# Kernel tuning notes

Measured on AMD Instinct MI355X. Metric: run time of the kernel, lower is better.

Reference implementation:

```python
import jax, jax.numpy as jnp
import numpy as np

N_NODES = 50000
N_EDGES = 800000
IN_DIM = 256
OUT_DIM = 256


def setup_inputs() -> dict:
    key = jax.random.key(0)
    k1, k2, k3, k4, k5, k6 = jax.random.split(key, 6)
    x = jax.random.normal(k1, (N_NODES, IN_DIM), dtype=jnp.float32)
    adj_rows = jax.random.randint(k2, (N_EDGES,), 0, N_NODES)
    adj_cols = jax.random.randint(k3, (N_EDGES,), 0, N_NODES)
    adj_vals = jax.random.uniform(k4, (N_EDGES,), dtype=jnp.float32)
    stdv = 1.0 / np.sqrt(OUT_DIM)
    W = jax.random.uniform(k5, (IN_DIM, OUT_DIM), minval=-stdv, maxval=stdv, dtype=jnp.float32)
    b = jax.random.uniform(k6, (OUT_DIM,), minval=-stdv, maxval=stdv, dtype=jnp.float32)
    return {"x": x, "adj_rows": adj_rows, "adj_cols": adj_cols, "adj_vals": adj_vals, "W": W, "b": b}


def reference(x, adj_rows, adj_cols, adj_vals, W, b):
    # hidden = x @ W  (first sparse.mm; x treated dense, identical math)
    hidden = jnp.matmul(x, W)  # [N, out_dim]
    # output = adj @ hidden via COO SpMM: gather source rows, scale, scatter-add to dest rows
    msgs = adj_vals[:, None] * hidden[adj_cols]  # [E, out_dim]
    output = jax.ops.segment_sum(msgs, adj_rows, num_segments=N_NODES)  # [N, out_dim]
    return output + b
```

## Files before the change

kernel.cpp:

```cpp
#include <hip/hip_runtime.h>

#define N_NODES 50000
#define N_EDGES 800000
#define DIM     256
#define STRIPS32 1563
#define NBLK_NODES 196
#define GEMM_BLOCKS 196
#define COUNT_BLOCKS 782
#define K2_BLOCKS (GEMM_BLOCKS + COUNT_BLOCKS)

typedef __attribute__((ext_vector_type(8))) short bf16x8;
typedef __attribute__((ext_vector_type(4))) float f32x4;

__device__ __forceinline__ unsigned short f2bf(float f) {
    unsigned u = __float_as_uint(f);
    unsigned r = (u + 0x7fffu + ((u >> 16) & 1u)) >> 16;
    return (unsigned short)r;
}
__device__ __forceinline__ float bf2f(unsigned short h) {
    return __uint_as_float((unsigned)h << 16);
}

__device__ __forceinline__ int block_excl_scan_256(int v, int* wsum, int* total) {
    const int lane = threadIdx.x & 63;
    const int wave = threadIdx.x >> 6;
    int x = v;
#pragma unroll
    for (int off = 1; off < 64; off <<= 1) {
        const int y = __shfl_up(x, off, 64);
        if (lane >= off) x += y;
    }
    if (lane == 63) wsum[wave] = x;
    __syncthreads();
    if (threadIdx.x == 0) {
        int s = 0;
#pragma unroll
        for (int w = 0; w < 4; ++w) { const int t = wsum[w]; wsum[w] = s; s += t; }
        *total = s;
    }
    __syncthreads();
    return wsum[wave] + x - v;
}

__global__ __launch_bounds__(256)
void prep(const float* __restrict__ W, unsigned short* __restrict__ Wt,
          int* __restrict__ cntcur) {
    const int i = blockIdx.x * 256 + threadIdx.x;
    if (i < 2 * N_NODES) cntcur[i] = 0;
    if (blockIdx.x < DIM) {
        const int n = blockIdx.x, k = threadIdx.x;
        Wt[n * DIM + k] = f2bf(W[(size_t)k * DIM + n]);
    }
}

__global__ __launch_bounds__(512, 2)
void gemm_count(const float* __restrict__ X, const unsigned short* __restrict__ Wt,
                unsigned short* __restrict__ Hb,
                const int* __restrict__ rows, int* __restrict__ cnt) {
    __shared__ unsigned short wl[DIM * DIM];
    const int tid = threadIdx.x;

    if (blockIdx.x >= GEMM_BLOCKS) {
        const int base = (blockIdx.x - GEMM_BLOCKS) * 1024;
        int e = base + tid;
        if (e < N_EDGES) atomicAdd(&cnt[rows[e]], 1);
        e += 512;
        if (e < N_EDGES) atomicAdd(&cnt[rows[e]], 1);
        return;
    }

    {
        const uint4* src = (const uint4*)Wt;
#pragma unroll
        for (int i = 0; i < 16; ++i) {
            const int c   = i * 512 + tid;
            const int row = c >> 5;
            const int kb  = (c & 31) * 16;
            const int dst = row * 512 + (kb ^ ((row & 7) << 4));
            *(uint4*)((char*)wl + dst) = src[c];
        }
    }
    __syncthreads();

    const int wid   = tid >> 6;
    const int lane  = tid & 63;
    const int strip = blockIdx.x * 8 + wid;
    if (strip >= STRIPS32) return;

    const int r0   = strip * 32;
    const int arow = lane & 15;
    const int kgrp = lane >> 4;
    const int ra = r0 + arow;
    const int rb = r0 + 16 + arow;
    const float* xa = X + (size_t)(ra < N_NODES ? ra : N_NODES - 1) * DIM + kgrp * 8;
    const float* xb = X + (size_t)(rb < N_NODES ? rb : N_NODES - 1) * DIM + kgrp * 8;

    f32x4 acc[2][16];
#pragma unroll
    for (int h = 0; h < 2; ++h)
#pragma unroll
        for (int nt = 0; nt < 16; ++nt) acc[h][nt] = f32x4{0.f, 0.f, 0.f, 0.f};

    const int swz = (arow & 7) << 4;

    float4 pa0 = *(const float4*)(xa);
    float4 pa1 = *(const float4*)(xa + 4);
    float4 pb0 = *(const float4*)(xb);
    float4 pb1 = *(const float4*)(xb + 4);

#pragma unroll
    for (int ks = 0; ks < 8; ++ks) {
        bf16x8 a0, a1;
        a0[0] = (short)f2bf(pa0.x); a0[1] = (short)f2bf(pa0.y);
        a0[2] = (short)f2bf(pa0.z); a0[3] = (short)f2bf(pa0.w);
        a0[4] = (short)f2bf(pa1.x); a0[5] = (short)f2bf(pa1.y);
        a0[6] = (short)f2bf(pa1.z); a0[7] = (short)f2bf(pa1.w);
        a1[0] = (short)f2bf(pb0.x); a1[1] = (short)f2bf(pb0.y);
        a1[2] = (short)f2bf(pb0.z); a1[3] = (short)f2bf(pb0.w);
        a1[4] = (short)f2bf(pb1.x); a1[5] = (short)f2bf(pb1.y);
        a1[6] = (short)f2bf(pb1.z); a1[7] = (short)f2bf(pb1.w);
        if (ks < 7) {
            pa0 = *(const float4*)(xa + (ks + 1) * 32);
            pa1 = *(const float4*)(xa + (ks + 1) * 32 + 4);
            pb0 = *(const float4*)(xb + (ks + 1) * 32);
            pb1 = *(const float4*)(xb + (ks + 1) * 32 + 4);
        }
        const int kb = ((ks * 32 + kgrp * 8) * 2) ^ swz;
#pragma unroll
        for (int nt = 0; nt < 16; ++nt) {
            const int n = nt * 16 + arow;
            const bf16x8 b = *(const bf16x8*)((const char*)wl + n * 512 + kb);
            acc[0][nt] = __builtin_amdgcn_mfma_f32_16x16x32_bf16(a0, b, acc[0][nt], 0, 0, 0);
            acc[1][nt] = __builtin_amdgcn_mfma_f32_16x16x32_bf16(a1, b, acc[1][nt], 0, 0, 0);
        }
    }

#pragma unroll
    for (int h = 0; h < 2; ++h) {
        const int crow0 = r0 + h * 16 + kgrp * 4;
#pragma unroll
        for (int nt = 0; nt < 16; ++nt) {
#pragma unroll
            for (int q = 0; q < 4; ++q) {
                const int r = crow0 + q;
                if (r < N_NODES)
                    Hb[(size_t)r * DIM + nt * 16 + arow] = f2bf(acc[h][nt][q]);
            }
        }
    }
}

__global__ __launch_bounds__(256)
void scan_blocks(const int* __restrict__ cnt, int* __restrict__ offs,
                 int* __restrict__ bsum) {
    __shared__ int wsum[4];
    __shared__ int total;
    const int i = blockIdx.x * 256 + threadIdx.x;
    const int v = (i < N_NODES) ? cnt[i] : 0;
    const int excl = block_excl_scan_256(v, wsum, &total);
    if (i < N_NODES) offs[i] = excl;
    if (threadIdx.x == 0) bsum[blockIdx.x] = total;
}

__global__ __launch_bounds__(256)
void fill_edges(const int* __restrict__ rows, const int* __restrict__ cols,
                const float* __restrict__ vals, const int* __restrict__ offs,
                const int* __restrict__ bsum, int* __restrict__ cursor,
                int2* __restrict__ pe) {
    __shared__ int wsum[4];
    __shared__ int total;
    __shared__ int P[256];
    {
        const int t = threadIdx.x;
        const int v = (t < NBLK_NODES) ? bsum[t] : 0;
        const int excl = block_excl_scan_256(v, wsum, &total);
        P[t] = excl;
    }
    __syncthreads();
    const int e = blockIdx.x * 256 + threadIdx.x;
    if (e >= N_EDGES) return;
    const int r = rows[e];
    const int p = atomicAdd(&cursor[r], 1);
    pe[offs[r] + P[r >> 8] + p] = make_int2(cols[e], __float_as_int(vals[e]));
}

__global__ __launch_bounds__(256)
void spmm(const unsigned short* __restrict__ Hb, const int* __restrict__ offs,
          const int* __restrict__ bsum, const int2* __restrict__ pe,
          const float* __restrict__ bias, float* __restrict__ out) {
    __shared__ int wsum[4];
    __shared__ int total;
    __shared__ int P[256];
    {
        const int t = threadIdx.x;
        const int v = (t < NBLK_NODES) ? bsum[t] : 0;
        const int excl = block_excl_scan_256(v, wsum, &total);
        P[t] = excl;
    }
    __syncthreads();

    const int row  = blockIdx.x * 4 + (threadIdx.x >> 6);
    const int lane = threadIdx.x & 63;
    const int beg = offs[row] + P[row >> 8];
    const int end = (row + 1 == N_NODES) ? N_EDGES : (offs[row + 1] + P[(row + 1) >> 8]);
    const unsigned lb = (unsigned)lane * 4;
    float4 acc = make_float4(0.f, 0.f, 0.f, 0.f);
    int i = beg;
    for (; i + 8 <= end; i += 8) {
        int2 e[8];
#pragma unroll
        for (int j = 0; j < 8; ++j) e[j] = pe[i + j];
        ushort4 h[8];
#pragma unroll
        for (int j = 0; j < 8; ++j)
            h[j] = *(const ushort4*)&Hb[((unsigned)e[j].x << 8) + lb];
#pragma unroll
        for (int j = 0; j < 8; ++j) {
            const float v = __int_as_float(e[j].y);
            acc.x += v * bf2f(h[j].x);
            acc.y += v * bf2f(h[j].y);
            acc.z += v * bf2f(h[j].z);
            acc.w += v * bf2f(h[j].w);
        }
    }
    for (; i < end; ++i) {
        const int2 e0 = pe[i];
        const ushort4 h0 = *(const ushort4*)&Hb[((unsigned)e0.x << 8) + lb];
        const float v0 = __int_as_float(e0.y);
        acc.x += v0 * bf2f(h0.x);
        acc.y += v0 * bf2f(h0.y);
        acc.z += v0 * bf2f(h0.z);
        acc.w += v0 * bf2f(h0.w);
    }
    const float4 bb = *(const float4*)&bias[lane * 4];
    acc.x += bb.x; acc.y += bb.y; acc.z += bb.z; acc.w += bb.w;
    *(float4*)&out[(size_t)row * DIM + lane * 4] = acc;
}

extern "C" void kernel_launch(void* const* d_in, const int* in_sizes, int n_in,
                              void* d_out, int out_size, void* d_ws, size_t ws_size,
                              hipStream_t stream) {
    const float* x        = (const float*)d_in[0];
    const int*   adj_rows = (const int*)d_in[1];
    const int*   adj_cols = (const int*)d_in[2];
    const float* adj_vals = (const float*)d_in[3];
    const float* W        = (const float*)d_in[4];
    const float* b        = (const float*)d_in[5];
    float*       out      = (float*)d_out;

    char* ws = (char*)d_ws;
    size_t off = 0;
    auto alloc = [&](size_t bytes) {
        void* p = ws + off;
        off = (off + bytes + 255) & ~(size_t)255;
        return p;
    };
    unsigned short* hiddenb = (unsigned short*)alloc((size_t)N_NODES * DIM * sizeof(unsigned short));
    unsigned short* Wt      = (unsigned short*)alloc((size_t)DIM * DIM * sizeof(unsigned short));
    int*   offs    = (int*)  alloc((size_t)N_NODES * sizeof(int));
    int*   cntcur  = (int*)  alloc((size_t)2 * N_NODES * sizeof(int));
    int*   bsum    = (int*)  alloc(256 * sizeof(int));
    int2*  pe      = (int2*) alloc((size_t)N_EDGES * sizeof(int2));
    int* cnt    = cntcur;
    int* cursor = cntcur + N_NODES;

    prep<<<(2 * N_NODES + 255) / 256, 256, 0, stream>>>(W, Wt, cntcur);

    gemm_count<<<K2_BLOCKS, 512, 0, stream>>>(x, Wt, hiddenb, adj_rows, cnt);

    scan_blocks<<<NBLK_NODES, 256, 0, stream>>>(cnt, offs, bsum);

    fill_edges<<<(N_EDGES + 255) / 256, 256, 0, stream>>>(
        adj_rows, adj_cols, adj_vals, offs, bsum, cursor, pe);

    spmm<<<N_NODES / 4, 256, 0, stream>>>(hiddenb, offs, bsum, pe, b, out);
}
```

Measured before the change: 249.1 us.

## Record per-edge atomic rank during counting to remove second atomic pass

The edge-count kernel now stores the value returned by each atomicAdd as a per-edge rank. fill_edges uses that rank directly instead of doing a second round of atomics on a cursor array. Counting is split out of the fused GEMM launch into its own vectorized kernel, and prep no longer zeroes the cursor. This removes contended atomics from fill_edges, at the cost of an extra rank buffer, a separate launch and losing overlap between counting and the GEMM.

Result: no change. 245.3 us (-1.5%).

```diff
diff --git a/kernel.cpp b/kernel.cpp
--- a/kernel.cpp
+++ b/kernel.cpp
@@ -6,8 +6,6 @@
 #define STRIPS32 1563
 #define NBLK_NODES 196
 #define GEMM_BLOCKS 196
-#define COUNT_BLOCKS 782
-#define K2_BLOCKS (GEMM_BLOCKS + COUNT_BLOCKS)
 
 typedef __attribute__((ext_vector_type(8))) short bf16x8;
 typedef __attribute__((ext_vector_type(4))) float f32x4;
@@ -44,31 +42,18 @@
 
 __global__ __launch_bounds__(256)
 void prep(const float* __restrict__ W, unsigned short* __restrict__ Wt,
-          int* __restrict__ cntcur) {
+          int* __restrict__ cnt) {
     const int i = blockIdx.x * 256 + threadIdx.x;
-    if (i < 2 * N_NODES) cntcur[i] = 0;
-    if (blockIdx.x < DIM) {
-        const int n = blockIdx.x, k = threadIdx.x;
-        Wt[n * DIM + k] = f2bf(W[(size_t)k * DIM + n]);
-    }
+    if (i < N_NODES) cnt[i] = 0;
+    const int n = blockIdx.x, k = threadIdx.x;
+    Wt[n * DIM + k] = f2bf(W[(size_t)k * DIM + n]);
 }
 
 __global__ __launch_bounds__(512, 2)
-void gemm_count(const float* __restrict__ X, const unsigned short* __restrict__ Wt,
-                unsigned short* __restrict__ Hb,
-                const int* __restrict__ rows, int* __restrict__ cnt) {
+void gemm_mfma(const float* __restrict__ X, const unsigned short* __restrict__ Wt,
+               unsigned short* __restrict__ Hb) {
     __shared__ unsigned short wl[DIM * DIM];
     const int tid = threadIdx.x;
-
-    if (blockIdx.x >= GEMM_BLOCKS) {
-        const int base = (blockIdx.x - GEMM_BLOCKS) * 1024;
-        int e = base + tid;
-        if (e < N_EDGES) atomicAdd(&cnt[rows[e]], 1);
-        e += 512;
-        if (e < N_EDGES) atomicAdd(&cnt[rows[e]], 1);
-        return;
-    }
-
     {
         const uint4* src = (const uint4*)Wt;
 #pragma unroll
@@ -151,6 +136,20 @@
 }
 
 __global__ __launch_bounds__(256)
+void count_rank(const int* __restrict__ rows, int* __restrict__ cnt,
+                unsigned short* __restrict__ rank) {
+    const int e0 = (blockIdx.x * 256 + threadIdx.x) * 4;
+    if (e0 >= N_EDGES) return;
+    const int4 r4 = *(const int4*)&rows[e0];
+    ushort4 rk;
+    rk.x = (unsigned short)atomicAdd(&cnt[r4.x], 1);
+    rk.y = (unsigned short)atomicAdd(&cnt[r4.y], 1);
+    rk.z = (unsigned short)atomicAdd(&cnt[r4.z], 1);
+    rk.w = (unsigned short)atomicAdd(&cnt[r4.w], 1);
+    *(ushort4*)&rank[e0] = rk;
+}
+
+__global__ __launch_bounds__(256)
 void scan_blocks(const int* __restrict__ cnt, int* __restrict__ offs,
                  int* __restrict__ bsum) {
     __shared__ int wsum[4];
@@ -165,7 +164,7 @@
 __global__ __launch_bounds__(256)
 void fill_edges(const int* __restrict__ rows, const int* __restrict__ cols,
                 const float* __restrict__ vals, const int* __restrict__ offs,
-                const int* __restrict__ bsum, int* __restrict__ cursor,
+                const int* __restrict__ bsum, const unsigned short* __restrict__ rank,
                 int2* __restrict__ pe) {
     __shared__ int wsum[4];
     __shared__ int total;
@@ -180,8 +179,7 @@
     const int e = blockIdx.x * 256 + threadIdx.x;
     if (e >= N_EDGES) return;
     const int r = rows[e];
-    const int p = atomicAdd(&cursor[r], 1);
-    pe[offs[r] + P[r >> 8] + p] = make_int2(cols[e], __float_as_int(vals[e]));
+    pe[offs[r] + P[r >> 8] + rank[e]] = make_int2(cols[e], __float_as_int(vals[e]));
 }
 
 __global__ __launch_bounds__(256)
@@ -257,21 +255,22 @@
     };
     unsigned short* hiddenb = (unsigned short*)alloc((size_t)N_NODES * DIM * sizeof(unsigned short));
     unsigned short* Wt      = (unsigned short*)alloc((size_t)DIM * DIM * sizeof(unsigned short));
-    int*   offs    = (int*)  alloc((size_t)N_NODES * sizeof(int));
-    int*   cntcur  = (int*)  alloc((size_t)2 * N_NODES * sizeof(int));
-    int*   bsum    = (int*)  alloc(256 * sizeof(int));
-    int2*  pe      = (int2*) alloc((size_t)N_EDGES * sizeof(int2));
-    int* cnt    = cntcur;
-    int* cursor = cntcur + N_NODES;
-
-    prep<<<(2 * N_NODES + 255) / 256, 256, 0, stream>>>(W, Wt, cntcur);
-
-    gemm_count<<<K2_BLOCKS, 512, 0, stream>>>(x, Wt, hiddenb, adj_rows, cnt);
+    int*            offs    = (int*)alloc((size_t)N_NODES * sizeof(int));
+    int*            cnt     = (int*)alloc((size_t)N_NODES * sizeof(int));
+    int*            bsum    = (int*)alloc(256 * sizeof(int));
+    unsigned short* rank    = (unsigned short*)alloc((size_t)N_EDGES * sizeof(unsigned short));
+    int2*           pe      = (int2*)alloc((size_t)N_EDGES * sizeof(int2));
+
+    prep<<<DIM, 256, 0, stream>>>(W, Wt, cnt);
+
+    gemm_mfma<<<GEMM_BLOCKS, 512, 0, stream>>>(x, Wt, hiddenb);
+
+    count_rank<<<(N_EDGES / 4 + 255) / 256, 256, 0, stream>>>(adj_rows, cnt, rank);
 
     scan_blocks<<<NBLK_NODES, 256, 0, stream>>>(cnt, offs, bsum);
 
     fill_edges<<<(N_EDGES + 255) / 256, 256, 0, stream>>>(
-        adj_rows, adj_cols, adj_vals, offs, bsum, cursor, pe);
+        adj_rows, adj_cols, adj_vals, offs, bsum, rank, pe);
 
     spmm<<<N_NODES / 4, 256, 0, stream>>>(hiddenb, offs, bsum, pe, b, out);
 }
```
